# Kernel optimization log

Hardware: AMD Instinct MI355X
Metric: run time of the kernel (lower is better)

## Reference

```python
import jax, jax.numpy as jnp
import numpy as np

N_NODES = 100000
N_EDGES = 1600000
IN_FEAT = 128
HIDDEN = 64
OUT_EMB = 64
N_GRAPHS = 256
PD_EPS = 1e-6  # torch PairwiseDistance eps added to the difference


def gcn_conv(x, src, dst, W, b):
    """PyG GCNConv: h = x@W, add self-loops, sym-normalized scatter-add, + bias."""
    n = x.shape[0]
    h = x @ W  # [N, out]
    loops = jnp.arange(n)
    s = jnp.concatenate([src, loops])
    d = jnp.concatenate([dst, loops])
    deg = jnp.zeros((n,), h.dtype).at[d].add(1.0)
    dinv = jnp.where(deg > 0, jax.lax.rsqrt(jnp.maximum(deg, 1.0)), 0.0)
    norm = (dinv[s] * dinv[d])[:, None]  # [E+N, 1]
    out = jnp.zeros_like(h).at[d].add(norm * h[s])  # gather + scatter-add
    return out + b


def mean_pool(x, batch, num_graphs):
    s = jax.ops.segment_sum(x, batch, num_segments=num_graphs)
    cnt = jax.ops.segment_sum(jnp.ones((x.shape[0],), x.dtype), batch,
                              num_segments=num_graphs)
    return s / jnp.maximum(cnt, 1.0)[:, None]


def tower(x, edge_index, batch, params, num_graphs):
    W1, b1, W2, b2, W3, b3, Wlin, blin = params
    src, dst = edge_index[0], edge_index[1]
    x = jax.nn.relu(gcn_conv(x, src, dst, W1, b1))
    x = jax.nn.relu(gcn_conv(x, src, dst, W2, b2))
    x = gcn_conv(x, src, dst, W3, b3)
    x = mean_pool(x, batch, num_graphs)
    # dropout omitted for determinism (eval mode)
    return x @ Wlin + blin


def setup_inputs() -> dict:
    key = jax.random.key(0)
    ks = jax.random.split(key, 16)

    def glorot(k, fan_in, fan_out):
        lim = np.sqrt(6.0 / (fan_in + fan_out))
        return jax.random.uniform(k, (fan_in, fan_out), jnp.float32, -lim, lim)

    return {
        "x1": jax.random.normal(ks[0], (N_NODES, IN_FEAT), jnp.float32),
        "edge_index1": jax.random.randint(ks[1], (2, N_EDGES), 0, N_NODES),
        "batch1": jnp.sort(jax.random.randint(ks[2], (N_NODES,), 0, N_GRAPHS)),
        "x2": jax.random.normal(ks[3], (N_NODES, IN_FEAT), jnp.float32),
        "edge_index2": jax.random.randint(ks[4], (2, N_EDGES), 0, N_NODES),
        "batch2": jnp.sort(jax.random.randint(ks[5], (N_NODES,), 0, N_GRAPHS)),
        "W1": glorot(ks[6], IN_FEAT, HIDDEN),
        "b1": jnp.zeros((HIDDEN,), jnp.float32),
        "W2": glorot(ks[7], HIDDEN, HIDDEN),
        "b2": jnp.zeros((HIDDEN,), jnp.float32),
        "W3": glorot(ks[8], HIDDEN, HIDDEN),
        "b3": jnp.zeros((HIDDEN,), jnp.float32),
        "Wlin": glorot(ks[9], HIDDEN, OUT_EMB),
        "blin": jnp.zeros((OUT_EMB,), jnp.float32),
        "num_graphs": N_GRAPHS,
    }


def reference(x1, edge_index1, batch1, x2, edge_index2, batch2,
              W1, b1, W2, b2, W3, b3, Wlin, blin, num_graphs):
    params = (W1, b1, W2, b2, W3, b3, Wlin, blin)
    e1 = tower(x1, edge_index1, batch1, params, num_graphs)  # [G, OUT_EMB]
    e2 = tower(x2, edge_index2, batch2, params, num_graphs)
    diff = e1 - e2 + PD_EPS
    return jnp.sqrt(jnp.sum(diff * diff, axis=-1))  # L2 PairwiseDistance, [G]
```

## Files before the change

### kernel.cpp

```cpp
#include <hip/hip_runtime.h>
#include <hip/hip_bf16.h>
#include <math.h>

#define NGRAPHS 256
#define PD_EPS 1e-6f
#define POOL_CHUNK 64
#define NCOLOR 16
#define CSHIFT 4
#define KB 96

typedef __hip_bfloat16 bf16;
typedef unsigned short ushort_t;
typedef short bf8_t __attribute__((ext_vector_type(8)));
typedef float f4_t __attribute__((ext_vector_type(4)));

static __device__ __forceinline__ int wave_uniform(int v) {
  return __builtin_amdgcn_readfirstlane(v);
}
static __device__ __forceinline__ float b2f(bf16 h) { return __bfloat162float(h); }
static __device__ __forceinline__ bf16 f2b(float f) { return __float2bfloat16(f); }
static __device__ __forceinline__ short f2bbits(float f) {
  bf16 h = __float2bfloat16(f);
  return *reinterpret_cast<short*>(&h);
}

__global__ __launch_bounds__(256) void k_count_part(const int* __restrict__ dst,
                                                    ushort_t* __restrict__ partial,
                                                    int E, int n, int rng) {
  extern __shared__ int hist[];
  int color = blockIdx.x & (NCOLOR - 1);
  int sub = blockIdx.x >> CSHIFT;
  int base = color * rng;
  int hi = n - base; if (hi > rng) hi = rng;
  for (int i = threadIdx.x; i < rng; i += 256) hist[i] = 0;
  __syncthreads();
  const int stride = KB * 256;
  int e = sub * 256 + threadIdx.x;
  for (; e + 7 * stride < E; e += 8 * stride) {
    int d[8];
#pragma unroll
    for (int k = 0; k < 8; ++k) d[k] = dst[e + k * stride] - base;
#pragma unroll
    for (int k = 0; k < 8; ++k)
      if ((unsigned)d[k] < (unsigned)hi) atomicAdd(&hist[d[k]], 1);
  }
  for (; e < E; e += stride) {
    int d = dst[e] - base;
    if ((unsigned)d < (unsigned)hi) atomicAdd(&hist[d], 1);
  }
  __syncthreads();
  ushort_t* outp = partial + (size_t)blockIdx.x * rng;
  for (int i = threadIdx.x; i < rng; i += 256) outp[i] = (ushort_t)hist[i];
}

__global__ void k_reduce_part(ushort_t* __restrict__ partial, int* __restrict__ cnt,
                              float* __restrict__ dinv, int n, int rng) {
  int i = blockIdx.x * 256 + threadIdx.x;
  if (i >= n) return;
  int c = i / rng, li = i - c * rng;
  int acc = 0;
  for (int s = 0; s < KB; ++s) {
    size_t idx = (size_t)(s * NCOLOR + c) * rng + li;
    int t = partial[idx];
    partial[idx] = (ushort_t)acc;
    acc += t;
  }
  cnt[i] = acc;
  dinv[i] = 1.0f / sqrtf((float)(acc + 1));
}

__global__ void k_scan1(const int* __restrict__ cnt, int* __restrict__ off,
                        int* __restrict__ bsums, int n) {
  __shared__ int s[256];
  int tid = threadIdx.x;
  int gid = blockIdx.x * 256 + tid;
  int v = (gid < n) ? cnt[gid] : 0;
  s[tid] = v; __syncthreads();
  for (int o = 1; o < 256; o <<= 1) {
    int t = (tid >= o) ? s[tid - o] : 0;
    __syncthreads();
    s[tid] += t;
    __syncthreads();
  }
  if (gid < n) off[gid] = s[tid] - v;
  if (tid == 255) bsums[blockIdx.x] = s[255];
}

__global__ void k_scan2(int* __restrict__ bsums, int nb) {
  __shared__ int s[512];
  int tid = threadIdx.x;
  int v = (tid < nb) ? bsums[tid] : 0;
  s[tid] = v; __syncthreads();
  for (int o = 1; o < 512; o <<= 1) {
    int t = (tid >= o) ? s[tid - o] : 0;
    __syncthreads();
    s[tid] += t;
    __syncthreads();
  }
  if (tid < nb) bsums[tid] = s[tid] - v;
}

__global__ void k_off_final(int* __restrict__ off, const int* __restrict__ bsums,
                            int n, int E) {
  int gid = blockIdx.x * 256 + threadIdx.x;
  if (gid < n) off[gid] += bsums[blockIdx.x];
  if (gid == 0) off[n] = E;
}

__global__ __launch_bounds__(256) void k_fill_col(const int* __restrict__ src,
                                                  const int* __restrict__ dst,
                                                  const int* __restrict__ off,
                                                  const ushort_t* __restrict__ partial,
                                                  int* __restrict__ csr, int E, int n,
                                                  int rng) {
  extern __shared__ int cur[];
  int color = blockIdx.x & (NCOLOR - 1);
  int sub = blockIdx.x >> CSHIFT;
  int base = color * rng;
  int hi = n - base; if (hi > rng) hi = rng;
  const ushort_t* pp = partial + (size_t)blockIdx.x * rng;
  for (int i = threadIdx.x; i < hi; i += 256) cur[i] = off[base + i] + (int)pp[i];
  __syncthreads();
  const int stride = KB * 256;
  int e = sub * 256 + threadIdx.x;
  for (; e + 7 * stride < E; e += 8 * stride) {
    int d[8], s[8];
#pragma unroll
    for (int k = 0; k < 8; ++k) d[k] = dst[e + k * stride] - base;
#pragma unroll
    for (int k = 0; k < 8; ++k) s[k] = src[e + k * stride];
#pragma unroll
    for (int k = 0; k < 8; ++k) {
      if ((unsigned)d[k] < (unsigned)hi) {
        int p = atomicAdd(&cur[d[k]], 1);
        csr[p] = s[k];
      }
    }
  }
  for (; e < E; e += stride) {
    int d = dst[e] - base;
    if ((unsigned)d < (unsigned)hi) {
      int p = atomicAdd(&cur[d], 1);
      csr[p] = src[e];
    }
  }
}

template <int K, int INF32>
__global__ __launch_bounds__(256, 2) void k_gemm_mfma(const void* __restrict__ inv,
                                                      const float* __restrict__ Wg,
                                                      const float* __restrict__ dinv,
                                                      bf16* __restrict__ out, int n) {
  constexpr int KS = K / 32;
  int lane = threadIdx.x & 63;
  int quad = lane >> 4;
  int col = lane & 15;

  bf8_t bfrag[4][KS];
#pragma unroll
  for (int c = 0; c < 4; ++c)
#pragma unroll
    for (int s = 0; s < KS; ++s)
#pragma unroll
      for (int j = 0; j < 8; ++j)
        bfrag[c][s][j] = f2bbits(Wg[(s * 32 + quad * 8 + j) * 64 + c * 16 + col]);

  int wid = (blockIdx.x * blockDim.x + threadIdx.x) >> 6;
  int nw = (gridDim.x * blockDim.x) >> 6;
  int tiles = (n + 15) >> 4;
  for (int t = wid; t < tiles; t += nw) {
    int base = t << 4;
    int arow = base + col;
    if (arow >= n) arow = n - 1;

    bf8_t afrag[KS];
    if (INF32) {
      const float* xr = (const float*)inv + (size_t)arow * K;
#pragma unroll
      for (int s = 0; s < KS; ++s) {
        float4 u0 = *(const float4*)(xr + s * 32 + quad * 8);
        float4 u1 = *(const float4*)(xr + s * 32 + quad * 8 + 4);
        afrag[s][0] = f2bbits(u0.x);
        afrag[s][1] = f2bbits(u0.y);
        afrag[s][2] = f2bbits(u0.z);
        afrag[s][3] = f2bbits(u0.w);
        afrag[s][4] = f2bbits(u1.x);
        afrag[s][5] = f2bbits(u1.y);
        afrag[s][6] = f2bbits(u1.z);
        afrag[s][7] = f2bbits(u1.w);
      }
    } else {
      const bf16* xr = (const bf16*)inv + (size_t)arow * K;
#pragma unroll
      for (int s = 0; s < KS; ++s)
        afrag[s] = *(const bf8_t*)(xr + s * 32 + quad * 8);
    }

    f4_t acc[4];
#pragma unroll
    for (int c = 0; c < 4; ++c) acc[c] = (f4_t){0.f, 0.f, 0.f, 0.f};
#pragma unroll
    for (int s = 0; s < KS; ++s)
#pragma unroll
      for (int c = 0; c < 4; ++c)
        acc[c] = __builtin_amdgcn_mfma_f32_16x16x32_bf16(afrag[s], bfrag[c][s],
                                                         acc[c], 0, 0, 0);
#pragma unroll
    for (int r = 0; r < 4; ++r) {
      int row = base + quad * 4 + r;
      if (row < n) {
        float sc = dinv[row];
#pragma unroll
        for (int c = 0; c < 4; ++c)
          out[(size_t)row * 64 + c * 16 + col] = f2b(acc[c][r] * sc);
      }
    }
  }
}

template <int OUTF32>
__global__ __launch_bounds__(256) void k_agg(const bf16* __restrict__ hp,
                                             const int* __restrict__ off,
                                             const int* __restrict__ csr,
                                             const float* __restrict__ dinv,
                                             const float* __restrict__ bias,
                                             void* __restrict__ outv, int n,
                                             int do_relu) {
  int lane = threadIdx.x & 63;
  int wid = (blockIdx.x * blockDim.x + threadIdx.x) >> 6;
  int nw = (gridDim.x * blockDim.x) >> 6;
  float b = bias[lane];
  for (int node = wid; node < n; node += nw) {
    int un = wave_uniform(node);
    int beg = off[un], end = off[un + 1];
    float acc = b2f(hp[(size_t)un * 64 + lane]);
    int e = beg;
    int efull = beg + ((end - beg) & ~7);
    for (; e < efull; e += 8) {
      int s0 = csr[e + 0], s1 = csr[e + 1], s2 = csr[e + 2], s3 = csr[e + 3];
      int s4 = csr[e + 4], s5 = csr[e + 5], s6 = csr[e + 6], s7 = csr[e + 7];
      float a0 = b2f(hp[(size_t)s0 * 64 + lane]);
      float a1 = b2f(hp[(size_t)s1 * 64 + lane]);
      float a2 = b2f(hp[(size_t)s2 * 64 + lane]);
      float a3 = b2f(hp[(size_t)s3 * 64 + lane]);
      float a4 = b2f(hp[(size_t)s4 * 64 + lane]);
      float a5 = b2f(hp[(size_t)s5 * 64 + lane]);
      float a6 = b2f(hp[(size_t)s6 * 64 + lane]);
      float a7 = b2f(hp[(size_t)s7 * 64 + lane]);
      acc += ((a0 + a1) + (a2 + a3)) + ((a4 + a5) + (a6 + a7));
    }
    int rem = end - e;
    if (rem & 4) {
      int s0 = csr[e + 0], s1 = csr[e + 1], s2 = csr[e + 2], s3 = csr[e + 3];
      float a0 = b2f(hp[(size_t)s0 * 64 + lane]);
      float a1 = b2f(hp[(size_t)s1 * 64 + lane]);
      float a2 = b2f(hp[(size_t)s2 * 64 + lane]);
      float a3 = b2f(hp[(size_t)s3 * 64 + lane]);
      acc += (a0 + a1) + (a2 + a3);
      e += 4;
    }
    if (rem & 2) {
      int s0 = csr[e + 0], s1 = csr[e + 1];
      float a0 = b2f(hp[(size_t)s0 * 64 + lane]);
      float a1 = b2f(hp[(size_t)s1 * 64 + lane]);
      acc += a0 + a1;
      e += 2;
    }
    if (rem & 1) {
      acc += b2f(hp[(size_t)csr[e] * 64 + lane]);
    }
    float v = fmaf(acc, dinv[un], b);
    if (do_relu) v = fmaxf(v, 0.f);
    if (OUTF32)
      ((float*)outv)[(size_t)un * 64 + lane] = v;
    else
      ((bf16*)outv)[(size_t)un * 64 + lane] = f2b(v);
  }
}

__global__ __launch_bounds__(256) void k_pool(const float* __restrict__ x3,
                                              const int* __restrict__ batch,
                                              float* __restrict__ pooled,
                                              float* __restrict__ cnt, int n) {
  int lane = threadIdx.x & 63;
  int wid = (blockIdx.x * blockDim.x + threadIdx.x) >> 6;
  int beg = wid * POOL_CHUNK;
  if (beg >= n) return;
  int end = beg + POOL_CHUNK;
  if (end > n) end = n;

  int cur = wave_uniform(batch[beg]);
  float acc = 0.f;
  int cl = 0;
  int i = beg;
  for (; i + 4 <= end; i += 4) {
    int g0 = wave_uniform(batch[i + 0]);
    int g3 = wave_uniform(batch[i + 3]);
    float a0 = x3[(size_t)(i + 0) * 64 + lane];
    float a1 = x3[(size_t)(i + 1) * 64 + lane];
    float a2 = x3[(size_t)(i + 2) * 64 + lane];
    float a3 = x3[(size_t)(i + 3) * 64 + lane];
    if (g0 == cur && g3 == cur) {
      acc += a0 + a1 + a2 + a3;
      cl += 4;
    } else {
      float av[4] = {a0, a1, a2, a3};
#pragma unroll
      for (int k = 0; k < 4; ++k) {
        int g = wave_uniform(batch[i + k]);
        if (g != cur) {
          atomicAdd(&pooled[cur * 64 + lane], acc);
          if (lane == 0) atomicAdd(&cnt[cur], (float)cl);
          acc = 0.f; cl = 0; cur = g;
        }
        acc += av[k];
        cl += 1;
      }
    }
  }
  for (; i < end; ++i) {
    int g = wave_uniform(batch[i]);
    float a = x3[(size_t)i * 64 + lane];
    if (g != cur) {
      atomicAdd(&pooled[cur * 64 + lane], acc);
      if (lane == 0) atomicAdd(&cnt[cur], (float)cl);
      acc = 0.f; cl = 0; cur = g;
    }
    acc += a;
    cl += 1;
  }
  atomicAdd(&pooled[cur * 64 + lane], acc);
  if (lane == 0) atomicAdd(&cnt[cur], (float)cl);
}

__global__ void k_final(const float* __restrict__ pooled1, const float* __restrict__ cnt1,
                        const float* __restrict__ pooled2, const float* __restrict__ cnt2,
                        const float* __restrict__ Wlin, const float* __restrict__ blin,
                        float* __restrict__ outp) {
  int g = blockIdx.x;
  int lane = threadIdx.x;
  float c1 = fmaxf(cnt1[g], 1.f), c2 = fmaxf(cnt2[g], 1.f);
  float p1 = pooled1[g * 64 + lane] / c1;
  float p2 = pooled2[g * 64 + lane] / c2;
  float e1 = blin[lane], e2 = blin[lane];
  for (int j = 0; j < 64; ++j) {
    float w = Wlin[j * 64 + lane];
    e1 = fmaf(__shfl(p1, j), w, e1);
    e2 = fmaf(__shfl(p2, j), w, e2);
  }
  float d = e1 - e2 + PD_EPS;
  float sq = d * d;
  for (int o = 32; o > 0; o >>= 1) sq += __shfl_down(sq, o);
  if (lane == 0) outp[g] = sqrtf(sq);
}

extern "C" void kernel_launch(void* const* d_in, const int* in_sizes, int n_in,
                              void* d_out, int out_size, void* d_ws, size_t ws_size,
                              hipStream_t stream) {
  const float* x1 = (const float*)d_in[0];
  const int* ei1 = (const int*)d_in[1];
  const int* batch1 = (const int*)d_in[2];
  const float* x2 = (const float*)d_in[3];
  const int* ei2 = (const int*)d_in[4];
  const int* batch2 = (const int*)d_in[5];
  const float* W1 = (const float*)d_in[6];
  const float* b1 = (const float*)d_in[7];
  const float* W2 = (const float*)d_in[8];
  const float* b2 = (const float*)d_in[9];
  const float* W3 = (const float*)d_in[10];
  const float* b3 = (const float*)d_in[11];
  const float* Wlin = (const float*)d_in[12];
  const float* blin = (const float*)d_in[13];

  const int N = in_sizes[2];
  const int E = in_sizes[1] / 2;
  const int rng = (N + NCOLOR - 1) / NCOLOR;

  char* p = (char*)d_ws;
  auto alloc = [&](size_t bytes) {
    char* r = p;
    p += (bytes + 255) & ~(size_t)255;
    return r;
  };
  int* off = (int*)alloc((size_t)(N + 1) * 4);
  int* cntn = (int*)alloc((size_t)N * 4);
  int* bsums = (int*)alloc(512 * 4);
  float* dinv = (float*)alloc((size_t)N * 4);
  int* csr = (int*)alloc((size_t)E * 4);
  char* unionbuf = alloc((size_t)N * 64 * 4);
  ushort_t* partial = (ushort_t*)unionbuf;
  float* bufF = (float*)unionbuf;
  bf16* hpA = (bf16*)alloc((size_t)N * 64 * 2);
  bf16* hpB = (bf16*)alloc((size_t)N * 64 * 2);
  float* pooled1 = (float*)alloc((size_t)NGRAPHS * 64 * 4);
  float* cnt1 = (float*)alloc((size_t)NGRAPHS * 4);
  float* pooled2 = (float*)alloc((size_t)NGRAPHS * 64 * 4);
  float* cnt2 = (float*)alloc((size_t)NGRAPHS * 4);

  const int nbN = (N + 255) / 256;
  const size_t ldsB = (size_t)rng * 4;

  for (int t = 0; t < 2; ++t) {
    const float* x = t ? x2 : x1;
    const int* src = t ? ei2 : ei1;
    const int* dst = src + E;
    const int* batch = t ? batch2 : batch1;
    float* pooled = t ? pooled2 : pooled1;
    float* cnt = t ? cnt2 : cnt1;

    hipMemsetAsync(pooled, 0, (size_t)NGRAPHS * 64 * 4, stream);
    hipMemsetAsync(cnt, 0, (size_t)NGRAPHS * 4, stream);

    k_count_part<<<NCOLOR * KB, 256, ldsB, stream>>>(dst, partial, E, N, rng);
    k_reduce_part<<<nbN, 256, 0, stream>>>(partial, cntn, dinv, N, rng);
    k_scan1<<<nbN, 256, 0, stream>>>(cntn, off, bsums, N);
    k_scan2<<<1, 512, 0, stream>>>(bsums, nbN);
    k_off_final<<<nbN, 256, 0, stream>>>(off, bsums, N, E);
    k_fill_col<<<NCOLOR * KB, 256, ldsB, stream>>>(src, dst, off, partial, csr, E, N,
                                                   rng);

    k_gemm_mfma<128, 1><<<512, 256, 0, stream>>>(x, W1, dinv, hpA, N);
    k_agg<0><<<2048, 256, 0, stream>>>(hpA, off, csr, dinv, b1, hpB, N, 1);
    k_gemm_mfma<64, 0><<<512, 256, 0, stream>>>(hpB, W2, dinv, hpA, N);
    k_agg<0><<<2048, 256, 0, stream>>>(hpA, off, csr, dinv, b2, hpB, N, 1);
    k_gemm_mfma<64, 0><<<512, 256, 0, stream>>>(hpB, W3, dinv, hpA, N);
    k_agg<1><<<2048, 256, 0, stream>>>(hpA, off, csr, dinv, b3, bufF, N, 0);

    const int poolWaves = (N + POOL_CHUNK - 1) / POOL_CHUNK;
    k_pool<<<(poolWaves + 3) / 4, 256, 0, stream>>>(bufF, batch, pooled, cnt, N);
  }
  k_final<<<NGRAPHS, 64, 0, stream>>>(pooled1, cnt1, pooled2, cnt2, Wlin, blin,
                                      (float*)d_out);
}
```

Measured before the change: 605.7 us.

## Defer layer-3 weight multiply past aggregation and mean pooling into final kernel

Because aggregation and mean pooling are linear, the third GCN layer's x@W3 is moved after pooling. Only 256 graph vectors are multiplied by W3 in k_final, and the per-node GEMM launch is removed. Layer 2's aggregation now pre-scales its output by dinv so layer 3 can aggregate directly. The per-tower memsets are merged into one. This relies on the bias being added after pooling, which is exact because every node's normalization sums consistently, though bf16 rounding happens at a different point.

```diff
diff --git a/kernel.cpp b/kernel.cpp
--- a/kernel.cpp
+++ b/kernel.cpp
@@ -218,18 +218,17 @@
   }
 }
 
-template <int OUTF32>
+template <int MODE>
 __global__ __launch_bounds__(256) void k_agg(const bf16* __restrict__ hp,
                                              const int* __restrict__ off,
                                              const int* __restrict__ csr,
                                              const float* __restrict__ dinv,
                                              const float* __restrict__ bias,
-                                             void* __restrict__ outv, int n,
-                                             int do_relu) {
+                                             void* __restrict__ outv, int n) {
   int lane = threadIdx.x & 63;
   int wid = (blockIdx.x * blockDim.x + threadIdx.x) >> 6;
   int nw = (gridDim.x * blockDim.x) >> 6;
-  float b = bias[lane];
+  float b = (MODE == 2) ? 0.f : bias[lane];
   for (int node = wid; node < n; node += nw) {
     int un = wave_uniform(node);
     int beg = off[un], end = off[un + 1];
@@ -269,12 +268,15 @@
     if (rem & 1) {
       acc += b2f(hp[(size_t)csr[e] * 64 + lane]);
     }
-    float v = fmaf(acc, dinv[un], b);
-    if (do_relu) v = fmaxf(v, 0.f);
-    if (OUTF32)
-      ((float*)outv)[(size_t)un * 64 + lane] = v;
-    else
+    float di = dinv[un];
+    if (MODE == 2) {
+      ((float*)outv)[(size_t)un * 64 + lane] = acc * di;
+    } else {
+      float v = fmaf(acc, di, b);
+      v = fmaxf(v, 0.f);
+      if (MODE == 1) v *= di;
       ((bf16*)outv)[(size_t)un * 64 + lane] = f2b(v);
+    }
   }
 }
 
@@ -335,6 +337,7 @@
 
 __global__ void k_final(const float* __restrict__ pooled1, const float* __restrict__ cnt1,
                         const float* __restrict__ pooled2, const float* __restrict__ cnt2,
+                        const float* __restrict__ W3, const float* __restrict__ b3,
                         const float* __restrict__ Wlin, const float* __restrict__ blin,
                         float* __restrict__ outp) {
   int g = blockIdx.x;
@@ -342,11 +345,17 @@
   float c1 = fmaxf(cnt1[g], 1.f), c2 = fmaxf(cnt2[g], 1.f);
   float p1 = pooled1[g * 64 + lane] / c1;
   float p2 = pooled2[g * 64 + lane] / c2;
+  float q1 = b3[lane], q2 = b3[lane];
+  for (int j = 0; j < 64; ++j) {
+    float w = W3[j * 64 + lane];
+    q1 = fmaf(__shfl(p1, j), w, q1);
+    q2 = fmaf(__shfl(p2, j), w, q2);
+  }
   float e1 = blin[lane], e2 = blin[lane];
   for (int j = 0; j < 64; ++j) {
     float w = Wlin[j * 64 + lane];
-    e1 = fmaf(__shfl(p1, j), w, e1);
-    e2 = fmaf(__shfl(p2, j), w, e2);
+    e1 = fmaf(__shfl(q1, j), w, e1);
+    e2 = fmaf(__shfl(q2, j), w, e2);
   }
   float d = e1 - e2 + PD_EPS;
   float sq = d * d;
@@ -396,9 +405,12 @@
   float* cnt1 = (float*)alloc((size_t)NGRAPHS * 4);
   float* pooled2 = (float*)alloc((size_t)NGRAPHS * 64 * 4);
   float* cnt2 = (float*)alloc((size_t)NGRAPHS * 4);
+  size_t poolspan = (size_t)((char*)(cnt2 + NGRAPHS) - (char*)pooled1);
 
   const int nbN = (N + 255) / 256;
   const size_t ldsB = (size_t)rng * 4;
+
+  hipMemsetAsync(pooled1, 0, poolspan, stream);
 
   for (int t = 0; t < 2; ++t) {
     const float* x = t ? x2 : x1;
@@ -408,9 +420,6 @@
     float* pooled = t ? pooled2 : pooled1;
     float* cnt = t ? cnt2 : cnt1;
 
-    hipMemsetAsync(pooled, 0, (size_t)NGRAPHS * 64 * 4, stream);
-    hipMemsetAsync(cnt, 0, (size_t)NGRAPHS * 4, stream);
-
     k_count_part<<<NCOLOR * KB, 256, ldsB, stream>>>(dst, partial, E, N, rng);
     k_reduce_part<<<nbN, 256, 0, stream>>>(partial, cntn, dinv, N, rng);
     k_scan1<<<nbN, 256, 0, stream>>>(cntn, off, bsums, N);
@@ -420,15 +429,14 @@
                                                    rng);
 
     k_gemm_mfma<128, 1><<<512, 256, 0, stream>>>(x, W1, dinv, hpA, N);
-    k_agg<0><<<2048, 256, 0, stream>>>(hpA, off, csr, dinv, b1, hpB, N, 1);
+    k_agg<0><<<2048, 256, 0, stream>>>(hpA, off, csr, dinv, b1, hpB, N);
     k_gemm_mfma<64, 0><<<512, 256, 0, stream>>>(hpB, W2, dinv, hpA, N);
-    k_agg<0><<<2048, 256, 0, stream>>>(hpA, off, csr, dinv, b2, hpB, N, 1);
-    k_gemm_mfma<64, 0><<<512, 256, 0, stream>>>(hpB, W3, dinv, hpA, N);
-    k_agg<1><<<2048, 256, 0, stream>>>(hpA, off, csr, dinv, b3, bufF, N, 0);
+    k_agg<1><<<2048, 256, 0, stream>>>(hpA, off, csr, dinv, b2, hpB, N);
+    k_agg<2><<<2048, 256, 0, stream>>>(hpB, off, csr, dinv, b3, bufF, N);
 
     const int poolWaves = (N + POOL_CHUNK - 1) / POOL_CHUNK;
     k_pool<<<(poolWaves + 3) / 4, 256, 0, stream>>>(bufF, batch, pooled, cnt, N);
   }
-  k_final<<<NGRAPHS, 64, 0, stream>>>(pooled1, cnt1, pooled2, cnt2, Wlin, blin,
-                                      (float*)d_out);
-}
+  k_final<<<NGRAPHS, 64, 0, stream>>>(pooled1, cnt1, pooled2, cnt2, W3, b3, Wlin,
+                                      blin, (float*)d_out);
+}
```

After: 580.6 us. 4.1% less time.
